# Kernel optimization log

Measured on AMD Instinct MI355X. Metric: run time of the kernel, lower is better.

## Reference

```python
import jax, jax.numpy as jnp
import numpy as np

MAX_LEN = 200
MAX_K = 3
ITERATION = 3
NEG_PAD = -2.0 ** 16 + 1.0


def setup_inputs() -> dict:
    key = jax.random.key(0)
    k1, k2, k3, k4 = jax.random.split(key, 4)
    B, L, D_in, D_out = 1024, MAX_LEN, 128, 128
    low_capsule = jax.random.normal(k1, (B, L, D_in), dtype=jnp.float32)
    B_matrix = jax.random.normal(k2, (1, MAX_K, L), dtype=jnp.float32)
    S_matrix = jax.random.normal(k3, (D_in, D_out), dtype=jnp.float32)
    # lengths in [1, MAX_LEN]; at least one row hits MAX_LEN so max(seq_len)==MAX_LEN
    seq_len = jax.random.randint(k4, (B, 1), 1, MAX_LEN + 1, dtype=jnp.int64)
    seq_len = seq_len.at[0, 0].set(MAX_LEN)
    return {"low_capsule": low_capsule, "B_matrix": B_matrix,
            "S_matrix": S_matrix, "seq_len": seq_len}


def squash(x):
    # torch code: norm over dim=1 (the capsule axis), keepdim
    sq = jnp.sum(jnp.square(x), axis=1, keepdims=True)
    scale = sq / (1.0 + sq) / jnp.sqrt(sq + 1e-9)
    return scale * x


def reference(low_capsule, B_matrix, S_matrix, seq_len):
    # low_capsule: [B, L, D_in], B_matrix: [1, K, L], S_matrix: [D_in, D_out], seq_len: [B, 1]
    # mask: [B, K, L] (seq_len tiled over K via broadcasting)
    mask = jnp.arange(MAX_LEN)[None, None, :] < seq_len[:, :, None]
    # bilinear projection is loop-invariant (same math as recomputing each iter)
    low_new = jnp.einsum('bld,de->ble', low_capsule, S_matrix)  # [B, L, D_out]
    high = None
    for _ in range(ITERATION):
        logits = jnp.where(mask, B_matrix, jnp.float32(NEG_PAD))  # [B, K, L]
        W = jax.nn.softmax(logits, axis=-1)
        high = squash(jnp.einsum('bkl,ble->bke', W, low_new))  # [B, K, D_out]
        # agreement, summed over batch with keepdim -> [1, K, L]
        B_delta = jnp.einsum('bke,ble->kl', high, low_new)[None]
        B_matrix = B_matrix + B_delta
    return high
```

## Files before the change

### kernel.cpp

```cpp
#include <hip/hip_runtime.h>
#include <math.h>

#define BATCH 1024
#define SEQ   200
#define DIN   128
#define DOUT  128
#define HALF  64
#define PSTR  608

typedef __attribute__((ext_vector_type(8))) short short8;
typedef __attribute__((ext_vector_type(4))) float f32x4;

__device__ __forceinline__ void async_copy16(const void* g, void* l) {
    __builtin_amdgcn_global_load_lds((const __attribute__((address_space(1))) void*)g,
                                     (__attribute__((address_space(3))) void*)l,
                                     16, 0, 0);
}

__device__ __forceinline__ unsigned pack_split(float f) {
    unsigned u = __float_as_uint(f);
    unsigned r = u + 0x8000u;
    unsigned hi = r >> 16;
    float hf = __uint_as_float(r & 0xffff0000u);
    unsigned lo = __float_as_uint(f - hf) >> 16;
    return (hi << 16) | lo;
}

__device__ __forceinline__ void split2(float f, short& h, short& l) {
    unsigned u = __float_as_uint(f);
    unsigned r = u + 0x8000u;
    h = (short)(r >> 16);
    float hf = __uint_as_float(r & 0xffff0000u);
    l = (short)(__float_as_uint(f - hf) >> 16);
}

__device__ __forceinline__ float unpk(unsigned u) {
    return __uint_as_float(u & 0xffff0000u) + __uint_as_float(u << 16);
}

__global__ __launch_bounds__(256) void k_presplit(const float* __restrict__ S,
                                                  short* __restrict__ Sp) {
    int g = blockIdx.x * 256 + threadIdx.x;
    int j = g & 7, lane = (g >> 3) & 63, kt = (g >> 9) & 3, nt = g >> 11;
    int k = kt * 32 + (lane >> 4) * 8 + j;
    int n = nt * 16 + (lane & 15);
    short h, l;
    split2(S[k * DOUT + n], h, l);
    Sp[g] = h;
    Sp[16384 + g] = l;
}

__global__ __launch_bounds__(256, 2) void k_gemm(const float* __restrict__ A,
                                                 const short* __restrict__ Sp,
                                                 unsigned* __restrict__ outp) {
    __shared__ short sSp[32768];
    const int t = threadIdx.x;
    const int w = t >> 6, lane = t & 63;
    const int q = lane >> 4, c = lane & 15;
    const long rowb = (long)blockIdx.x * 128 + w * 32;

    float4 araw[4][2][2];
#pragma unroll
    for (int kt = 0; kt < 4; ++kt)
#pragma unroll
        for (int mt = 0; mt < 2; ++mt) {
            const float* ap = A + (rowb + mt * 16 + c) * DIN + kt * 32 + q * 8;
            araw[kt][mt][0] = *(const float4*)ap;
            araw[kt][mt][1] = *(const float4*)(ap + 4);
        }

#pragma unroll
    for (int i = 0; i < 16; ++i) {
        const int g = w * 16 + i;
        async_copy16(Sp + g * 512 + lane * 8, &sSp[g * 512]);
    }

    short8 ah[4][2], al[4][2];
#pragma unroll
    for (int kt = 0; kt < 4; ++kt)
#pragma unroll
        for (int mt = 0; mt < 2; ++mt) {
            float av[8];
            *(float4*)&av[0] = araw[kt][mt][0];
            *(float4*)&av[4] = araw[kt][mt][1];
#pragma unroll
            for (int j = 0; j < 8; ++j) {
                short h, l;
                split2(av[j], h, l);
                ah[kt][mt][j] = h; al[kt][mt][j] = l;
            }
        }

    f32x4 acc[2][8];
    const f32x4 zz = {0.f, 0.f, 0.f, 0.f};
#pragma unroll
    for (int mt = 0; mt < 2; ++mt)
#pragma unroll
        for (int nt = 0; nt < 8; ++nt) acc[mt][nt] = zz;

    __syncthreads();

#pragma unroll
    for (int kt = 0; kt < 4; ++kt)
#pragma unroll
        for (int nt = 0; nt < 8; ++nt) {
            const int fo = ((nt * 4 + kt) * 64 + lane) * 8;
            short8 sh = *(const short8*)&sSp[fo];
            short8 sl = *(const short8*)&sSp[16384 + fo];
#pragma unroll
            for (int mt = 0; mt < 2; ++mt) {
                acc[mt][nt] = __builtin_amdgcn_mfma_f32_16x16x32_bf16(ah[kt][mt], sh, acc[mt][nt], 0, 0, 0);
                acc[mt][nt] = __builtin_amdgcn_mfma_f32_16x16x32_bf16(al[kt][mt], sh, acc[mt][nt], 0, 0, 0);
                acc[mt][nt] = __builtin_amdgcn_mfma_f32_16x16x32_bf16(ah[kt][mt], sl, acc[mt][nt], 0, 0, 0);
            }
        }
#pragma unroll
    for (int mt = 0; mt < 2; ++mt)
#pragma unroll
        for (int nt = 0; nt < 8; ++nt) {
            long r0 = rowb + mt * 16 + q * 4;
#pragma unroll
            for (int r = 0; r < 4; ++r)
                outp[(r0 + r) * DOUT + nt * 16 + c] = pack_split(acc[mt][nt][r]);
        }
}

__global__ __launch_bounds__(256, 2) void k_iter(
    const unsigned* __restrict__ lowp,
    const float* __restrict__ Bm,
    const int* __restrict__ seq,
    const float* __restrict__ acc0, const float* __restrict__ acc1,
    float* __restrict__ part,
    float* __restrict__ out, int iter) {
    __shared__ unsigned sLn[SEQ * HALF];
    __shared__ float sW[SEQ * 4];
    __shared__ float pB[4][3][HALF];
    __shared__ float sH[3][HALF];

    const int t = threadIdx.x;
    const int lane = t & 63, w = t >> 6;
    const int b = blockIdx.x >> 1, half = blockIdx.x & 1;
    const unsigned* lp = lowp + (size_t)b * (SEQ * DIN) + half * HALF;
    const int n = seq[b];

    float a0v[4], a1v[4], a2v[4];
    if (w < 3) {
        const int k = w;
#pragma unroll
        for (int i = 0; i < 4; ++i) {
            int l = lane + 64 * i;
            bool inb = (l < SEQ);
            a0v[i] = inb ? Bm[k * SEQ + l] : 0.f;
            a1v[i] = (inb && iter >= 1) ? acc0[k * SEQ + l] : 0.f;
            a2v[i] = (inb && iter >= 2) ? acc1[k * SEQ + l] : 0.f;
        }
    }

    for (int g = w; g < 50; g += 4)
        async_copy16(lp + (g * 4 + (lane >> 4)) * DIN + (lane & 15) * 4,
                     &sLn[g * 256]);

    if (w < 3) {
        const int k = w;
        float vv[4], m = -INFINITY;
#pragma unroll
        for (int i = 0; i < 4; ++i) {
            int l = lane + 64 * i;
            float v = a0v[i] + a1v[i] + a2v[i];
            vv[i] = (l < n) ? v : -INFINITY;
            if (l < n) m = fmaxf(m, v);
        }
        for (int off = 32; off; off >>= 1) m = fmaxf(m, __shfl_xor(m, off, 64));
        float s = 0.f, pv[4];
#pragma unroll
        for (int i = 0; i < 4; ++i) {
            pv[i] = (vv[i] == -INFINITY) ? 0.f : expf(vv[i] - m);
            s += pv[i];
        }
        for (int off = 32; off; off >>= 1) s += __shfl_xor(s, off, 64);
        float rs = 1.f / s;
#pragma unroll
        for (int i = 0; i < 4; ++i) {
            int l = lane + 64 * i;
            if (l < SEQ) sW[l * 4 + k] = pv[i] * rs;
        }
    }
    __syncthreads();

    {
        const int e = lane;
        float h0 = 0.f, h1 = 0.f, h2 = 0.f;
        for (int i = 0; i < 50; ++i) {
            int l = w * 50 + i;
            float4 wv = *(const float4*)&sW[l * 4];
            float f = unpk(sLn[l * 64 + e]);
            h0 = fmaf(wv.x, f, h0);
            h1 = fmaf(wv.y, f, h1);
            h2 = fmaf(wv.z, f, h2);
        }
        pB[w][0][e] = h0; pB[w][1][e] = h1; pB[w][2][e] = h2;
    }
    __syncthreads();

    if (t < HALF) {
        float g0 = pB[0][0][t] + pB[1][0][t] + pB[2][0][t] + pB[3][0][t];
        float g1 = pB[0][1][t] + pB[1][1][t] + pB[2][1][t] + pB[3][1][t];
        float g2 = pB[0][2][t] + pB[1][2][t] + pB[2][2][t] + pB[3][2][t];
        float sq = g0 * g0 + g1 * g1 + g2 * g2;
        float scale = sq / (1.f + sq) / sqrtf(sq + 1e-9f);
        g0 *= scale; g1 *= scale; g2 *= scale;
        if (iter == 2) {
            size_t o = (size_t)b * 3 * DOUT + half * HALF + t;
            out[o] = g0; out[o + DOUT] = g1; out[o + 2 * DOUT] = g2;
        } else {
            sH[0][t] = g0; sH[1][t] = g1; sH[2][t] = g2;
        }
    }
    if (iter == 2) return;
    __syncthreads();

    if (t < SEQ) {
        const int l = t;
        float d0 = 0.f, d1 = 0.f, d2 = 0.f;
#pragma unroll
        for (int j = 0; j < 16; ++j) {
            const int jj = (j + l) & 15;
            uint4 u = *(const uint4*)&sLn[l * 64 + 4 * jj];
            float4 x0 = *(const float4*)&sH[0][4 * jj];
            float4 x1 = *(const float4*)&sH[1][4 * jj];
            float4 x2 = *(const float4*)&sH[2][4 * jj];
            float f0 = unpk(u.x), f1 = unpk(u.y), f2 = unpk(u.z), f3 = unpk(u.w);
            d0 += x0.x * f0 + x0.y * f1 + x0.z * f2 + x0.w * f3;
            d1 += x1.x * f0 + x1.y * f1 + x1.z * f2 + x1.w * f3;
            d2 += x2.x * f0 + x2.y * f1 + x2.z * f2 + x2.w * f3;
        }
        float* pp = part + (size_t)blockIdx.x * PSTR;
        pp[l] = d0;
        pp[SEQ + l] = d1;
        pp[2 * SEQ + l] = d2;
    }
}

__global__ __launch_bounds__(256) void k_reduce(const float* __restrict__ part,
                                                float* __restrict__ accN) {
    __shared__ float sP[4][4];
    const int t = threadIdx.x, lane = t & 63, w = t >> 6;
    const int c4 = blockIdx.x * 4;
    float sx = 0.f, sy = 0.f, sz = 0.f, sw = 0.f;
#pragma unroll
    for (int i = 0; i < 8; ++i) {
        float4 v = *(const float4*)&part[(size_t)(t + 256 * i) * PSTR + c4];
        sx += v.x; sy += v.y; sz += v.z; sw += v.w;
    }
#pragma unroll
    for (int off = 1; off < 64; off <<= 1) {
        sx += __shfl_xor(sx, off, 64);
        sy += __shfl_xor(sy, off, 64);
        sz += __shfl_xor(sz, off, 64);
        sw += __shfl_xor(sw, off, 64);
    }
    if (lane == 0) { sP[w][0] = sx; sP[w][1] = sy; sP[w][2] = sz; sP[w][3] = sw; }
    __syncthreads();
    if (t < 4)
        accN[c4 + t] = sP[0][t] + sP[1][t] + sP[2][t] + sP[3][t];
}

extern "C" void kernel_launch(void* const* d_in, const int* in_sizes, int n_in,
                              void* d_out, int out_size, void* d_ws, size_t ws_size,
                              hipStream_t stream) {
    const float* low_capsule = (const float*)d_in[0];
    const float* B_matrix    = (const float*)d_in[1];
    const float* S_matrix    = (const float*)d_in[2];
    const int*   seq_len     = (const int*)d_in[3];
    float* out = (float*)d_out;

    unsigned* lowp = (unsigned*)d_ws;
    short* Sp      = (short*)(lowp + (size_t)BATCH * SEQ * DOUT);
    float* acc0    = (float*)(Sp + 32768);
    float* acc1    = acc0 + 640;
    float* part    = acc1 + 640;

    k_presplit<<<64, 256, 0, stream>>>(S_matrix, Sp);
    k_gemm<<<(BATCH * SEQ) / 128, 256, 0, stream>>>(low_capsule, Sp, lowp);

    k_iter<<<2 * BATCH, 256, 0, stream>>>(lowp, B_matrix, seq_len, acc0, acc1, part, out, 0);
    k_reduce<<<150, 256, 0, stream>>>(part, acc0);
    k_iter<<<2 * BATCH, 256, 0, stream>>>(lowp, B_matrix, seq_len, acc0, acc1, part, out, 1);
    k_reduce<<<150, 256, 0, stream>>>(part, acc1);
    k_iter<<<2 * BATCH, 256, 0, stream>>>(lowp, B_matrix, seq_len, acc0, acc1, part, out, 2);
}
```

Measured before the change: 285.5 us.

## Drop LDS staging in routing kernel and widen GEMM blocks to 512 threads

```diff
diff --git a/kernel.cpp b/kernel.cpp
--- a/kernel.cpp
+++ b/kernel.cpp
@@ -50,14 +50,14 @@
     Sp[16384 + g] = l;
 }
 
-__global__ __launch_bounds__(256, 2) void k_gemm(const float* __restrict__ A,
+__global__ __launch_bounds__(512, 4) void k_gemm(const float* __restrict__ A,
                                                  const short* __restrict__ Sp,
                                                  unsigned* __restrict__ outp) {
     __shared__ short sSp[32768];
     const int t = threadIdx.x;
     const int w = t >> 6, lane = t & 63;
     const int q = lane >> 4, c = lane & 15;
-    const long rowb = (long)blockIdx.x * 128 + w * 32;
+    const long rowb = (long)blockIdx.x * 256 + w * 32;
 
     float4 araw[4][2][2];
 #pragma unroll
@@ -70,8 +70,8 @@
         }
 
 #pragma unroll
-    for (int i = 0; i < 16; ++i) {
-        const int g = w * 16 + i;
+    for (int i = 0; i < 8; ++i) {
+        const int g = w * 8 + i;
         async_copy16(Sp + g * 512 + lane * 8, &sSp[g * 512]);
     }
 
@@ -125,14 +125,13 @@
         }
 }
 
-__global__ __launch_bounds__(256, 2) void k_iter(
+__global__ __launch_bounds__(256, 6) void k_iter(
     const unsigned* __restrict__ lowp,
     const float* __restrict__ Bm,
     const int* __restrict__ seq,
     const float* __restrict__ acc0, const float* __restrict__ acc1,
     float* __restrict__ part,
     float* __restrict__ out, int iter) {
-    __shared__ unsigned sLn[SEQ * HALF];
     __shared__ float sW[SEQ * 4];
     __shared__ float pB[4][3][HALF];
     __shared__ float sH[3][HALF];
@@ -143,30 +142,16 @@
     const unsigned* lp = lowp + (size_t)b * (SEQ * DIN) + half * HALF;
     const int n = seq[b];
 
-    float a0v[4], a1v[4], a2v[4];
     if (w < 3) {
         const int k = w;
+        float vv[4], m = -INFINITY;
 #pragma unroll
         for (int i = 0; i < 4; ++i) {
             int l = lane + 64 * i;
             bool inb = (l < SEQ);
-            a0v[i] = inb ? Bm[k * SEQ + l] : 0.f;
-            a1v[i] = (inb && iter >= 1) ? acc0[k * SEQ + l] : 0.f;
-            a2v[i] = (inb && iter >= 2) ? acc1[k * SEQ + l] : 0.f;
-        }
-    }
-
-    for (int g = w; g < 50; g += 4)
-        async_copy16(lp + (g * 4 + (lane >> 4)) * DIN + (lane & 15) * 4,
-                     &sLn[g * 256]);
-
-    if (w < 3) {
-        const int k = w;
-        float vv[4], m = -INFINITY;
-#pragma unroll
-        for (int i = 0; i < 4; ++i) {
-            int l = lane + 64 * i;
-            float v = a0v[i] + a1v[i] + a2v[i];
+            float v = inb ? Bm[k * SEQ + l] : 0.f;
+            if (iter >= 1 && inb) v += acc0[k * SEQ + l];
+            if (iter >= 2 && inb) v += acc1[k * SEQ + l];
             vv[i] = (l < n) ? v : -INFINITY;
             if (l < n) m = fmaxf(m, v);
         }
@@ -189,11 +174,13 @@
 
     {
         const int e = lane;
+        const unsigned* col = lp + e;
         float h0 = 0.f, h1 = 0.f, h2 = 0.f;
+#pragma unroll 10
         for (int i = 0; i < 50; ++i) {
             int l = w * 50 + i;
             float4 wv = *(const float4*)&sW[l * 4];
-            float f = unpk(sLn[l * 64 + e]);
+            float f = unpk(col[(size_t)l * DIN]);
             h0 = fmaf(wv.x, f, h0);
             h1 = fmaf(wv.y, f, h1);
             h2 = fmaf(wv.z, f, h2);
@@ -221,14 +208,14 @@
 
     if (t < SEQ) {
         const int l = t;
+        const unsigned* row = lp + (size_t)l * DIN;
         float d0 = 0.f, d1 = 0.f, d2 = 0.f;
 #pragma unroll
         for (int j = 0; j < 16; ++j) {
-            const int jj = (j + l) & 15;
-            uint4 u = *(const uint4*)&sLn[l * 64 + 4 * jj];
-            float4 x0 = *(const float4*)&sH[0][4 * jj];
-            float4 x1 = *(const float4*)&sH[1][4 * jj];
-            float4 x2 = *(const float4*)&sH[2][4 * jj];
+            uint4 u = *(const uint4*)&row[4 * j];
+            float4 x0 = *(const float4*)&sH[0][4 * j];
+            float4 x1 = *(const float4*)&sH[1][4 * j];
+            float4 x2 = *(const float4*)&sH[2][4 * j];
             float f0 = unpk(u.x), f1 = unpk(u.y), f2 = unpk(u.z), f3 = unpk(u.w);
             d0 += x0.x * f0 + x0.y * f1 + x0.z * f2 + x0.w * f3;
             d1 += x1.x * f0 + x1.y * f1 + x1.z * f2 + x1.w * f3;
@@ -281,7 +268,7 @@
     float* part    = acc1 + 640;
 
     k_presplit<<<64, 256, 0, stream>>>(S_matrix, Sp);
-    k_gemm<<<(BATCH * SEQ) / 128, 256, 0, stream>>>(low_capsule, Sp, lowp);
+    k_gemm<<<(BATCH * SEQ) / 256, 512, 0, stream>>>(low_capsule, Sp, lowp);
 
     k_iter<<<2 * BATCH, 256, 0, stream>>>(lowp, B_matrix, seq_len, acc0, acc1, part, out, 0);
     k_reduce<<<150, 256, 0, stream>>>(part, acc0);
```

Result: slower. 299.1 us (+4.8%).
